# Kernel optimization log

Measured on AMD Instinct MI355X. Metric: run time of the kernel, lower is better.

Reference implementation:

```python
import jax, jax.numpy as jnp
import numpy as np

N_NODES = 50000
N_EDGES = 800000
F_IN = 64
HID = 64
OUT = 2
N_GRAPHS = 500


def _lin_init(key, fan_in, fan_out):
    # uniform(-1/sqrt(fan_in), 1/sqrt(fan_in)), matching torch Linear default
    bound = 1.0 / np.sqrt(fan_in)
    return jax.random.uniform(key, (fan_in, fan_out), minval=-bound, maxval=bound, dtype=jnp.float32)


def setup_inputs() -> dict:
    key = jax.random.key(0)
    ks = jax.random.split(key, 16)
    x = jax.random.normal(ks[0], (N_NODES, F_IN), dtype=jnp.float32)
    edge_index = jax.random.randint(ks[1], (2, N_EDGES), 0, N_NODES, dtype=jnp.int64)
    batch = jnp.sort(jax.random.randint(ks[2], (N_NODES,), 0, N_GRAPHS, dtype=jnp.int64))
    dims = [(F_IN, HID), (HID, HID), (HID, HID)]
    params = {}
    for i, (fi, fo) in enumerate(dims, start=1):
        params[f"W{i}_rel"] = _lin_init(ks[2 + 3 * i], fi, fo)      # applied to aggregated neighbors
        params[f"W{i}_root"] = _lin_init(ks[3 + 3 * i], fi, fo)     # applied to self (no bias, PyG GraphConv)
        b_bound = 1.0 / np.sqrt(fi)
        params[f"b{i}"] = jax.random.uniform(ks[4 + 3 * i], (fo,), minval=-b_bound, maxval=b_bound, dtype=jnp.float32)
    params["Wf1"] = _lin_init(ks[13], HID, HID)
    params["bf1"] = jnp.zeros((HID,), dtype=jnp.float32)
    params["Wf2"] = _lin_init(ks[14], HID, OUT)
    params["bf2"] = jnp.zeros((OUT,), dtype=jnp.float32)
    return {"x": x, "edge_index": edge_index, "batch": batch, **params}


def _graph_conv(h, src, dst, W_rel, W_root, b):
    # PyG GraphConv: out_i = W_root h_i + W_rel * sum_{j->i} h_j + b
    agg = jax.ops.segment_sum(h[src], dst, num_segments=N_NODES)  # [N, F] gather + scatter-add
    return h @ W_root + agg @ W_rel + b


def reference(x, edge_index, batch,
              W1_rel, W1_root, b1,
              W2_rel, W2_root, b2,
              W3_rel, W3_root, b3,
              Wf1, bf1, Wf2, bf2):
    src, dst = edge_index[0], edge_index[1]
    # dropout is identity in eval mode
    h = jax.nn.relu(_graph_conv(x, src, dst, W1_rel, W1_root, b1))
    h = jax.nn.relu(_graph_conv(h, src, dst, W2_rel, W2_root, b2))
    h = jax.nn.relu(_graph_conv(h, src, dst, W3_rel, W3_root, b3))
    # global_mean_pool over graph ids
    sums = jax.ops.segment_sum(h, batch, num_segments=N_GRAPHS)            # [G, H]
    counts = jax.ops.segment_sum(jnp.ones((N_NODES,), h.dtype), batch, num_segments=N_GRAPHS)
    pooled = sums / jnp.maximum(counts, 1.0)[:, None]
    out = pooled @ Wf1 + bf1
    out = out @ Wf2 + bf2
    return out
```

## Files before the change

### kernel.cpp

```cpp
#include <hip/hip_runtime.h>


#define NFEAT 64
#define BCAP  6144

typedef unsigned short u16;
typedef unsigned int   u32;
typedef __attribute__((ext_vector_type(8))) short short8;
typedef __attribute__((ext_vector_type(4))) float f32x4;

__device__ __forceinline__ u16 f2bf(float f) {
    u32 u = __float_as_uint(f);
    u32 r = (u + 0x7fffu + ((u >> 16) & 1u)) >> 16;
    return (u16)r;
}
__device__ __forceinline__ float bflo(u32 u) { return __uint_as_float(u << 16); }
__device__ __forceinline__ float bfhi(u32 u) { return __uint_as_float(u & 0xffff0000u); }

__global__ __launch_bounds__(256) void cast_bf(const float* __restrict__ in,
                                               u16* __restrict__ out, int n8) {
    int i = blockIdx.x * 256 + threadIdx.x;
    if (i < n8) {
        const float4* p = (const float4*)(in + (size_t)i * 8);
        float4 a = p[0], b = p[1];
        uint4 o;
        o.x = f2bf(a.x) | ((u32)f2bf(a.y) << 16);
        o.y = f2bf(a.z) | ((u32)f2bf(a.w) << 16);
        o.z = f2bf(b.x) | ((u32)f2bf(b.y) << 16);
        o.w = f2bf(b.z) | ((u32)f2bf(b.w) << 16);
        *(uint4*)(out + (size_t)i * 8) = o;
    }
}

__global__ __launch_bounds__(256) void gemm_cat(
    const u16* __restrict__ hin, const u16* __restrict__ agg,
    const float* __restrict__ Wroot, const float* __restrict__ Wrel,
    const float* __restrict__ bias, u16* __restrict__ hout, int n_rows)
{
    __shared__ u16 als[64 * 128];
    __shared__ u16 wls[64 * 128];

    const int tid = threadIdx.x;
    const int row0 = blockIdx.x * 64;

    #pragma unroll
    for (int it = 0; it < 4; ++it) {
        int id = it * 256 + tid;
        int k = id >> 4;
        int n4 = (id & 15) * 4;
        float4 wr = *(const float4*)(Wroot + k * 64 + n4);
        float4 wl = *(const float4*)(Wrel  + k * 64 + n4);
        const float* wrf = (const float*)&wr;
        const float* wlf = (const float*)&wl;
        int ckr = k >> 3, kin = k & 7;
        int ckl = ckr + 8;
        #pragma unroll
        for (int j = 0; j < 4; ++j) {
            int n = n4 + j;
            wls[n * 128 + (((ckr ^ (n & 7)) << 3) | kin)] = f2bf(wrf[j]);
            wls[n * 128 + (((ckl ^ (n & 7)) << 3) | kin)] = f2bf(wlf[j]);
        }
    }

    #pragma unroll
    for (int it = 0; it < 4; ++it) {
        int id = it * 256 + tid;
        int r = id >> 4, ch = id & 15;
        int gr = row0 + r;
        uint4 v = make_uint4(0, 0, 0, 0);
        if (gr < n_rows) {
            const u16* sp = (ch < 8) ? (hin + (size_t)gr * 64 + ch * 8)
                                     : (agg + (size_t)gr * 64 + (ch - 8) * 8);
            v = *(const uint4*)sp;
        }
        *(uint4*)&als[r * 128 + ((ch ^ (r & 7)) << 3)] = v;
    }
    __syncthreads();

    const int w = tid >> 6, l = tid & 63;
    const int l15 = l & 15;
    const int wrow0 = w * 16;

    short8 afr[4];
    #pragma unroll
    for (int ks = 0; ks < 4; ++ks) {
        int r = wrow0 + l15;
        int ck = ks * 4 + (l >> 4);
        afr[ks] = *(const short8*)&als[r * 128 + ((ck ^ (r & 7)) << 3)];
    }
    short8 bfr[4][4];
    #pragma unroll
    for (int nl = 0; nl < 4; ++nl)
        #pragma unroll
        for (int ks = 0; ks < 4; ++ks) {
            int cl = nl * 16 + l15;
            int ck = ks * 4 + (l >> 4);
            bfr[nl][ks] = *(const short8*)&wls[cl * 128 + ((ck ^ (cl & 7)) << 3)];
        }

    f32x4 acc[4];
    #pragma unroll
    for (int nl = 0; nl < 4; ++nl) {
        float bv = bias[nl * 16 + l15];
        f32x4 iv = {bv, bv, bv, bv};
        acc[nl] = iv;
    }
    #pragma unroll
    for (int nl = 0; nl < 4; ++nl)
        #pragma unroll
        for (int ks = 0; ks < 4; ++ks)
            acc[nl] = __builtin_amdgcn_mfma_f32_16x16x32_bf16(
                afr[ks], bfr[nl][ks], acc[nl], 0, 0, 0);

    const int rg = (l >> 4) * 4;
    #pragma unroll
    for (int reg = 0; reg < 4; ++reg) {
        int row = row0 + wrow0 + rg + reg;
        if (row < n_rows) {
            #pragma unroll
            for (int nl = 0; nl < 4; ++nl)
                hout[(size_t)row * 64 + nl * 16 + l15] =
                    f2bf(fmaxf(acc[nl][reg], 0.f));
        }
    }
}

__global__ __launch_bounds__(256) void zero_int(int* __restrict__ p, int n) {
    int i = blockIdx.x * 256 + threadIdx.x;
    if (i < n) p[i] = 0;
}

__global__ __launch_bounds__(256) void part_bucket(
    const int* __restrict__ src, const int* __restrict__ dst, int ne,
    int* __restrict__ bcnt, u32* __restrict__ pairs)
{
    __shared__ int lcnt[256];
    __shared__ int lbase[256];
    const int t = threadIdx.x;
    const int e0 = blockIdx.x * 4096;

    lcnt[t] = 0;
    __syncthreads();

    int s_[16], d_[16];
    #pragma unroll
    for (int i = 0; i < 16; ++i) {
        int e = e0 + i * 256 + t;
        if (e < ne) { s_[i] = src[e]; d_[i] = dst[e]; }
        else        { s_[i] = 0;      d_[i] = -1; }
    }
    #pragma unroll
    for (int i = 0; i < 16; ++i)
        if (d_[i] >= 0) atomicAdd(&lcnt[d_[i] >> 8], 1);
    __syncthreads();

    {
        int c = lcnt[t];
        lbase[t] = (c > 0) ? atomicAdd(&bcnt[t], c) : 0;
    }
    __syncthreads();
    lcnt[t] = 0;
    __syncthreads();

    #pragma unroll
    for (int i = 0; i < 16; ++i)
        if (d_[i] >= 0) {
            int b = d_[i] >> 8;
            int o = atomicAdd(&lcnt[b], 1);
            pairs[(size_t)b * BCAP + lbase[b] + o] =
                (u32)s_[i] | ((u32)(d_[i] & 255) << 16);
        }
}

__global__ __launch_bounds__(64) void scan_offsets(const int* __restrict__ bcnt, int nbuck,
                                                   int* __restrict__ boff,
                                                   int* __restrict__ row_ptr, int nn) {
    const int t = threadIdx.x;
    int carry = 0;
    for (int base = 0; base < nbuck; base += 64) {
        int i = base + t;
        int v = (i < nbuck) ? bcnt[i] : 0;
        int inc = v;
        #pragma unroll
        for (int off = 1; off < 64; off <<= 1) {
            int x = __shfl_up(inc, off);
            if (t >= off) inc += x;
        }
        if (i < nbuck) boff[i] = carry + inc - v;
        carry += __shfl(inc, 63);
    }
    if (t == 0) row_ptr[nn] = carry;
}

__global__ __launch_bounds__(256) void build_csr(
    const u32* __restrict__ pairs, const int* __restrict__ bcnt,
    const int* __restrict__ boff, int nn,
    int* __restrict__ row_ptr, u16* __restrict__ csr_src)
{
    __shared__ u32 lp[BCAP];
    __shared__ int deg[256];
    __shared__ int tsum[256];
    __shared__ int lofs[256];
    __shared__ int cur[256];

    const int b = blockIdx.x;
    const int t = threadIdx.x;
    const int cnt   = bcnt[b];
    const int ebase = boff[b];
    const int n0    = b * 256;

    deg[t] = 0; cur[t] = 0;
    __syncthreads();

    for (int i = t; i < cnt; i += 256) {
        u32 p = pairs[(size_t)b * BCAP + i];
        lp[i] = p;
        atomicAdd(&deg[p >> 16], 1);
    }
    __syncthreads();

    tsum[t] = deg[t];
    __syncthreads();
    #pragma unroll
    for (int off = 1; off < 256; off <<= 1) {
        int x = (t >= off) ? tsum[t - off] : 0;
        __syncthreads();
        tsum[t] += x;
        __syncthreads();
    }
    int excl = (t > 0 ? tsum[t - 1] : 0);
    lofs[t] = ebase + excl;
    int node = n0 + t;
    if (node < nn) row_ptr[node] = ebase + excl;
    __syncthreads();

    for (int i = t; i < cnt; i += 256) {
        u32 p = lp[i];
        int dl = p >> 16;
        int pos = lofs[dl] + atomicAdd(&cur[dl], 1);
        csr_src[pos] = (u16)(p & 0xffffu);
    }
}

__global__ __launch_bounds__(256) void gather_agg(
    const u16* __restrict__ hb,
    const int* __restrict__ row_ptr,
    const u16* __restrict__ csr_src,
    u16* __restrict__ agg,
    int nn)
{
    const int node = blockIdx.x * 4 + (threadIdx.x >> 6);
    const int l = threadIdx.x & 63;
    if (node >= nn) return;
    const int s = row_ptr[node];
    const int e = row_ptr[node + 1];
    const int es = l >> 3;
    const int c  = l & 7;
    const uint4* hv = (const uint4*)hb;

    float a0=0.f,a1=0.f,a2=0.f,a3=0.f,a4=0.f,a5=0.f,a6=0.f,a7=0.f;
    for (int j = s; j < e; j += 8) {
        int je = j + es;
        int jj = (je < e) ? je : (e - 1);
        float m = (je < e) ? 1.f : 0.f;
        int srcn = csr_src[jj];
        uint4 q = hv[(size_t)srcn * 8 + c];
        a0 = fmaf(m, bflo(q.x), a0);  a1 = fmaf(m, bfhi(q.x), a1);
        a2 = fmaf(m, bflo(q.y), a2);  a3 = fmaf(m, bfhi(q.y), a3);
        a4 = fmaf(m, bflo(q.z), a4);  a5 = fmaf(m, bfhi(q.z), a5);
        a6 = fmaf(m, bflo(q.w), a6);  a7 = fmaf(m, bfhi(q.w), a7);
    }
    #pragma unroll
    for (int msk = 8; msk <= 32; msk <<= 1) {
        a0 += __shfl_xor(a0, msk); a1 += __shfl_xor(a1, msk);
        a2 += __shfl_xor(a2, msk); a3 += __shfl_xor(a3, msk);
        a4 += __shfl_xor(a4, msk); a5 += __shfl_xor(a5, msk);
        a6 += __shfl_xor(a6, msk); a7 += __shfl_xor(a7, msk);
    }
    if (es == 0) {
        uint4 o;
        o.x = f2bf(a0) | ((u32)f2bf(a1) << 16);
        o.y = f2bf(a2) | ((u32)f2bf(a3) << 16);
        o.z = f2bf(a4) | ((u32)f2bf(a5) << 16);
        o.w = f2bf(a6) | ((u32)f2bf(a7) << 16);
        ((uint4*)agg)[(size_t)node * 8 + c] = o;
    }
}

__global__ __launch_bounds__(256) void pool_mlp(
    const u16* __restrict__ h,
    const int* __restrict__ batch,
    int n_nodes,
    const float* __restrict__ Wf1, const float* __restrict__ bf1,
    const float* __restrict__ Wf2, const float* __restrict__ bf2,
    float* __restrict__ out, int n_graphs)
{
    const int g = blockIdx.x;
    const int tid = threadIdx.x;

    int lo = 0, hi = n_nodes;
    while (lo < hi) { int mid = (lo + hi) >> 1; if (batch[mid] < g) lo = mid + 1; else hi = mid; }
    int s = lo;
    lo = s; hi = n_nodes;
    while (lo < hi) { int mid = (lo + hi) >> 1; if (batch[mid] < g + 1) lo = mid + 1; else hi = mid; }
    int e = lo;

    const int c16 = tid & 15;
    const int r16 = tid >> 4;
    const uint2* hv = (const uint2*)h;

    float4 acc = make_float4(0.f, 0.f, 0.f, 0.f);
    for (int i = s + r16; i < e; i += 16) {
        uint2 q = hv[(size_t)i * 16 + c16];
        acc.x += bflo(q.x); acc.y += bfhi(q.x);
        acc.z += bflo(q.y); acc.w += bfhi(q.y);
    }

    __shared__ float4 red[256];
    red[tid] = acc;
    __syncthreads();
    #pragma unroll
    for (int off = 8; off > 0; off >>= 1) {
        if (r16 < off) {
            float4 o = red[tid + off * 16];
            float4 m = red[tid];
            m.x += o.x; m.y += o.y; m.z += o.z; m.w += o.w;
            red[tid] = m;
        }
        __syncthreads();
    }

    __shared__ float pl[64];
    __shared__ float md[64];
    if (r16 == 0) {
        float inv = 1.0f / (float)((e - s) > 0 ? (e - s) : 1);
        float4 m = red[c16];
        pl[c16 * 4 + 0] = m.x * inv;
        pl[c16 * 4 + 1] = m.y * inv;
        pl[c16 * 4 + 2] = m.z * inv;
        pl[c16 * 4 + 3] = m.w * inv;
    }
    __syncthreads();

    if (tid < 64) {
        float m = bf1[tid];
        #pragma unroll 8
        for (int k = 0; k < 64; ++k)
            m += pl[k] * Wf1[k * 64 + tid];
        md[tid] = m;
    }
    __syncthreads();

    if (tid < 2) {
        float o = bf2[tid];
        #pragma unroll 8
        for (int k = 0; k < 64; ++k)
            o += md[k] * Wf2[k * 2 + tid];
        out[(size_t)g * 2 + tid] = o;
    }
}

extern "C" void kernel_launch(void* const* d_in, const int* in_sizes, int n_in,
                              void* d_out, int out_size, void* d_ws, size_t ws_size,
                              hipStream_t stream) {
    const float* x     = (const float*)d_in[0];
    const int*   ei    = (const int*)d_in[1];
    const int*   batch = (const int*)d_in[2];
    const float* W1_rel  = (const float*)d_in[3];
    const float* W1_root = (const float*)d_in[4];
    const float* b1      = (const float*)d_in[5];
    const float* W2_rel  = (const float*)d_in[6];
    const float* W2_root = (const float*)d_in[7];
    const float* b2      = (const float*)d_in[8];
    const float* W3_rel  = (const float*)d_in[9];
    const float* W3_root = (const float*)d_in[10];
    const float* b3      = (const float*)d_in[11];
    const float* Wf1     = (const float*)d_in[12];
    const float* bf1     = (const float*)d_in[13];
    const float* Wf2     = (const float*)d_in[14];
    const float* bf2     = (const float*)d_in[15];

    const int NN = in_sizes[0] / NFEAT;
    const int NE = in_sizes[1] / 2;
    const int NG = out_size / 2;

    const int* src = ei;
    const int* dst = ei + NE;

    const int nbuck = (NN + 255) / 256;

    u16*   hA      = (u16*)d_ws;
    u16*   hB      = hA + (size_t)NN * NFEAT;
    u16*   aggb    = hB + (size_t)NN * NFEAT;
    int*   row_ptr = (int*)(aggb + (size_t)NN * NFEAT);
    int*   bcnt    = row_ptr + (NN + 1);
    int*   boff    = bcnt + nbuck;
    u32*   pairs   = (u32*)(boff + nbuck);
    u16*   csr_src = (u16*)(pairs + (size_t)nbuck * BCAP);

    const int gemm_grid = (NN + 63) / 64;
    const int node_grid = (NN + 3) / 4;
    const int part_grid = (NE + 4095) / 4096;
    const int n8        = NN * NFEAT / 8;
    const int cast_grid = (n8 + 255) / 256;

    cast_bf<<<cast_grid, 256, 0, stream>>>(x, hB, n8);

    zero_int<<<(nbuck + 255) / 256, 256, 0, stream>>>(bcnt, nbuck);
    part_bucket<<<part_grid, 256, 0, stream>>>(src, dst, NE, bcnt, pairs);
    scan_offsets<<<1, 64, 0, stream>>>(bcnt, nbuck, boff, row_ptr, NN);
    build_csr<<<nbuck, 256, 0, stream>>>(pairs, bcnt, boff, NN, row_ptr, csr_src);

    gather_agg<<<node_grid, 256, 0, stream>>>(hB, row_ptr, csr_src, aggb, NN);
    gemm_cat<<<gemm_grid, 256, 0, stream>>>(hB, aggb, W1_root, W1_rel, b1, hA, NN);

    gather_agg<<<node_grid, 256, 0, stream>>>(hA, row_ptr, csr_src, aggb, NN);
    gemm_cat<<<gemm_grid, 256, 0, stream>>>(hA, aggb, W2_root, W2_rel, b2, hB, NN);

    gather_agg<<<node_grid, 256, 0, stream>>>(hB, row_ptr, csr_src, aggb, NN);
    gemm_cat<<<gemm_grid, 256, 0, stream>>>(hB, aggb, W3_root, W3_rel, b3, hA, NN);

    pool_mlp<<<NG, 256, 0, stream>>>(hA, batch, NN, Wf1, bf1, Wf2, bf2, (float*)d_out, NG);
}
```

Before: 142.4 us.

## Fuse neighbor gather-aggregation into the per-layer GEMM kernel via LDS

Merges the separate gather_agg and gemm_cat kernels into one layer_fused kernel. Each block now aggregates neighbor features for its 64 rows directly into the shared-memory A tile, so the intermediate agg buffer is never written to or read back from global memory. This also removes three kernel launches. The gather loop is unrolled to two edges per step for more memory-level parallelism. The cost is fewer waves in flight for the latency-bound gather: gemm_grid blocks each handle 16 nodes per wave in sequence, where before there were 4 nodes per block.

```diff
diff --git a/kernel.cpp b/kernel.cpp
--- a/kernel.cpp
+++ b/kernel.cpp
@@ -32,8 +32,10 @@
     }
 }
 
-__global__ __launch_bounds__(256) void gemm_cat(
-    const u16* __restrict__ hin, const u16* __restrict__ agg,
+__global__ __launch_bounds__(256) void layer_fused(
+    const u16* __restrict__ hin,
+    const int* __restrict__ row_ptr,
+    const u16* __restrict__ csr_src,
     const float* __restrict__ Wroot, const float* __restrict__ Wrel,
     const float* __restrict__ bias, u16* __restrict__ hout, int n_rows)
 {
@@ -63,17 +65,65 @@
     }
 
     #pragma unroll
-    for (int it = 0; it < 4; ++it) {
+    for (int it = 0; it < 2; ++it) {
         int id = it * 256 + tid;
-        int r = id >> 4, ch = id & 15;
+        int r = id >> 3, ch = id & 7;
         int gr = row0 + r;
         uint4 v = make_uint4(0, 0, 0, 0);
-        if (gr < n_rows) {
-            const u16* sp = (ch < 8) ? (hin + (size_t)gr * 64 + ch * 8)
-                                     : (agg + (size_t)gr * 64 + (ch - 8) * 8);
-            v = *(const uint4*)sp;
-        }
+        if (gr < n_rows) v = *(const uint4*)(hin + (size_t)gr * 64 + ch * 8);
         *(uint4*)&als[r * 128 + ((ch ^ (r & 7)) << 3)] = v;
+    }
+
+    {
+        const int w  = tid >> 6;
+        const int l  = tid & 63;
+        const int es = l >> 3;
+        const int c  = l & 7;
+        const uint4* hv = (const uint4*)hin;
+
+        for (int i = 0; i < 16; ++i) {
+            int r = w * 16 + i;
+            int node = row0 + r;
+            float a0=0.f,a1=0.f,a2=0.f,a3=0.f,a4=0.f,a5=0.f,a6=0.f,a7=0.f;
+            if (node < n_rows) {
+                const int s = row_ptr[node];
+                const int e = row_ptr[node + 1];
+                for (int j = s; j < e; j += 16) {
+                    int je0 = j + es, je1 = j + es + 8;
+                    int jj0 = (je0 < e) ? je0 : (e - 1);
+                    int jj1 = (je1 < e) ? je1 : (e - 1);
+                    float m0 = (je0 < e) ? 1.f : 0.f;
+                    float m1 = (je1 < e) ? 1.f : 0.f;
+                    int s0 = csr_src[jj0];
+                    int s1 = csr_src[jj1];
+                    uint4 q0 = hv[(size_t)s0 * 8 + c];
+                    uint4 q1 = hv[(size_t)s1 * 8 + c];
+                    a0 = fmaf(m0, bflo(q0.x), a0);  a1 = fmaf(m0, bfhi(q0.x), a1);
+                    a2 = fmaf(m0, bflo(q0.y), a2);  a3 = fmaf(m0, bfhi(q0.y), a3);
+                    a4 = fmaf(m0, bflo(q0.z), a4);  a5 = fmaf(m0, bfhi(q0.z), a5);
+                    a6 = fmaf(m0, bflo(q0.w), a6);  a7 = fmaf(m0, bfhi(q0.w), a7);
+                    a0 = fmaf(m1, bflo(q1.x), a0);  a1 = fmaf(m1, bfhi(q1.x), a1);
+                    a2 = fmaf(m1, bflo(q1.y), a2);  a3 = fmaf(m1, bfhi(q1.y), a3);
+                    a4 = fmaf(m1, bflo(q1.z), a4);  a5 = fmaf(m1, bfhi(q1.z), a5);
+                    a6 = fmaf(m1, bflo(q1.w), a6);  a7 = fmaf(m1, bfhi(q1.w), a7);
+                }
+            }
+            #pragma unroll
+            for (int msk = 8; msk <= 32; msk <<= 1) {
+                a0 += __shfl_xor(a0, msk); a1 += __shfl_xor(a1, msk);
+                a2 += __shfl_xor(a2, msk); a3 += __shfl_xor(a3, msk);
+                a4 += __shfl_xor(a4, msk); a5 += __shfl_xor(a5, msk);
+                a6 += __shfl_xor(a6, msk); a7 += __shfl_xor(a7, msk);
+            }
+            if (es == 0) {
+                uint4 o;
+                o.x = f2bf(a0) | ((u32)f2bf(a1) << 16);
+                o.y = f2bf(a2) | ((u32)f2bf(a3) << 16);
+                o.z = f2bf(a4) | ((u32)f2bf(a5) << 16);
+                o.w = f2bf(a6) | ((u32)f2bf(a7) << 16);
+                *(uint4*)&als[r * 128 + (((8 + c) ^ (r & 7)) << 3)] = o;
+            }
+        }
     }
     __syncthreads();
 
@@ -239,51 +289,6 @@
         int dl = p >> 16;
         int pos = lofs[dl] + atomicAdd(&cur[dl], 1);
         csr_src[pos] = (u16)(p & 0xffffu);
-    }
-}
-
-__global__ __launch_bounds__(256) void gather_agg(
-    const u16* __restrict__ hb,
-    const int* __restrict__ row_ptr,
-    const u16* __restrict__ csr_src,
-    u16* __restrict__ agg,
-    int nn)
-{
-    const int node = blockIdx.x * 4 + (threadIdx.x >> 6);
-    const int l = threadIdx.x & 63;
-    if (node >= nn) return;
-    const int s = row_ptr[node];
-    const int e = row_ptr[node + 1];
-    const int es = l >> 3;
-    const int c  = l & 7;
-    const uint4* hv = (const uint4*)hb;
-
-    float a0=0.f,a1=0.f,a2=0.f,a3=0.f,a4=0.f,a5=0.f,a6=0.f,a7=0.f;
-    for (int j = s; j < e; j += 8) {
-        int je = j + es;
-        int jj = (je < e) ? je : (e - 1);
-        float m = (je < e) ? 1.f : 0.f;
-        int srcn = csr_src[jj];
-        uint4 q = hv[(size_t)srcn * 8 + c];
-        a0 = fmaf(m, bflo(q.x), a0);  a1 = fmaf(m, bfhi(q.x), a1);
-        a2 = fmaf(m, bflo(q.y), a2);  a3 = fmaf(m, bfhi(q.y), a3);
-        a4 = fmaf(m, bflo(q.z), a4);  a5 = fmaf(m, bfhi(q.z), a5);
-        a6 = fmaf(m, bflo(q.w), a6);  a7 = fmaf(m, bfhi(q.w), a7);
-    }
-    #pragma unroll
-    for (int msk = 8; msk <= 32; msk <<= 1) {
-        a0 += __shfl_xor(a0, msk); a1 += __shfl_xor(a1, msk);
-        a2 += __shfl_xor(a2, msk); a3 += __shfl_xor(a3, msk);
-        a4 += __shfl_xor(a4, msk); a5 += __shfl_xor(a5, msk);
-        a6 += __shfl_xor(a6, msk); a7 += __shfl_xor(a7, msk);
-    }
-    if (es == 0) {
-        uint4 o;
-        o.x = f2bf(a0) | ((u32)f2bf(a1) << 16);
-        o.y = f2bf(a2) | ((u32)f2bf(a3) << 16);
-        o.z = f2bf(a4) | ((u32)f2bf(a5) << 16);
-        o.w = f2bf(a6) | ((u32)f2bf(a7) << 16);
-        ((uint4*)agg)[(size_t)node * 8 + c] = o;
     }
 }
 
@@ -391,15 +396,13 @@
 
     u16*   hA      = (u16*)d_ws;
     u16*   hB      = hA + (size_t)NN * NFEAT;
-    u16*   aggb    = hB + (size_t)NN * NFEAT;
-    int*   row_ptr = (int*)(aggb + (size_t)NN * NFEAT);
+    int*   row_ptr = (int*)(hB + (size_t)NN * NFEAT);
     int*   bcnt    = row_ptr + (NN + 1);
     int*   boff    = bcnt + nbuck;
     u32*   pairs   = (u32*)(boff + nbuck);
     u16*   csr_src = (u16*)(pairs + (size_t)nbuck * BCAP);
 
     const int gemm_grid = (NN + 63) / 64;
-    const int node_grid = (NN + 3) / 4;
     const int part_grid = (NE + 4095) / 4096;
     const int n8        = NN * NFEAT / 8;
     const int cast_grid = (n8 + 255) / 256;
@@ -411,14 +414,12 @@
     scan_offsets<<<1, 64, 0, stream>>>(bcnt, nbuck, boff, row_ptr, NN);
     build_csr<<<nbuck, 256, 0, stream>>>(pairs, bcnt, boff, NN, row_ptr, csr_src);
 
-    gather_agg<<<node_grid, 256, 0, stream>>>(hB, row_ptr, csr_src, aggb, NN);
-    gemm_cat<<<gemm_grid, 256, 0, stream>>>(hB, aggb, W1_root, W1_rel, b1, hA, NN);
-
-    gather_agg<<<node_grid, 256, 0, stream>>>(hA, row_ptr, csr_src, aggb, NN);
-    gemm_cat<<<gemm_grid, 256, 0, stream>>>(hA, aggb, W2_root, W2_rel, b2, hB, NN);
-
-    gather_agg<<<node_grid, 256, 0, stream>>>(hB, row_ptr, csr_src, aggb, NN);
-    gemm_cat<<<gemm_grid, 256, 0, stream>>>(hB, aggb, W3_root, W3_rel, b3, hA, NN);
+    layer_fused<<<gemm_grid, 256, 0, stream>>>(hB, row_ptr, csr_src,
+                                               W1_root, W1_rel, b1, hA, NN);
+    layer_fused<<<gemm_grid, 256, 0, stream>>>(hA, row_ptr, csr_src,
+                                               W2_root, W2_rel, b2, hB, NN);
+    layer_fused<<<gemm_grid, 256, 0, stream>>>(hB, row_ptr, csr_src,
+                                               W3_root, W3_rel, b3, hA, NN);
 
     pool_mlp<<<NG, 256, 0, stream>>>(hA, batch, NN, Wf1, bf1, Wf2, bf2, (float*)d_out, NG);
 }
```

Result: slower. 163.5 us (+14.8%).

## Fuse prep kernels, pre-swizzle bf16 weights once, unroll gather loop by two

Applied to the files above, without the earlier changes.

Merges the input cast, bucket-counter zeroing and a new weight-conversion step into one prep launch, removing a kernel launch. The three layers' weights are converted to bf16 in the swizzled LDS layout once, so each gemm_cat block now does a plain vector copy instead of per-block float loads, conversion and scattered LDS stores. The gather loop processes two edges per lane per iteration to keep more independent loads in flight. Costs are a small extra workspace region and a hardcoded CAST_BLKS that must cover n8 and assumes nbuck is at most 256.

```diff
diff --git a/kernel.cpp b/kernel.cpp
--- a/kernel.cpp
+++ b/kernel.cpp
@@ -17,25 +17,54 @@
 __device__ __forceinline__ float bflo(u32 u) { return __uint_as_float(u << 16); }
 __device__ __forceinline__ float bfhi(u32 u) { return __uint_as_float(u & 0xffff0000u); }
 
-__global__ __launch_bounds__(256) void cast_bf(const float* __restrict__ in,
-                                               u16* __restrict__ out, int n8) {
-    int i = blockIdx.x * 256 + threadIdx.x;
-    if (i < n8) {
-        const float4* p = (const float4*)(in + (size_t)i * 8);
-        float4 a = p[0], b = p[1];
-        uint4 o;
-        o.x = f2bf(a.x) | ((u32)f2bf(a.y) << 16);
-        o.y = f2bf(a.z) | ((u32)f2bf(a.w) << 16);
-        o.z = f2bf(b.x) | ((u32)f2bf(b.y) << 16);
-        o.w = f2bf(b.z) | ((u32)f2bf(b.w) << 16);
-        *(uint4*)(out + (size_t)i * 8) = o;
+#define CAST_BLKS 1600
+__global__ __launch_bounds__(256) void prep(
+    const float* __restrict__ x, u16* __restrict__ xb, int n8,
+    const float* __restrict__ W1r, const float* __restrict__ W1l,
+    const float* __restrict__ W2r, const float* __restrict__ W2l,
+    const float* __restrict__ W3r, const float* __restrict__ W3l,
+    u16* __restrict__ wimg, int* __restrict__ bcnt, int nbuck)
+{
+    const int bid = blockIdx.x;
+    const int tid = threadIdx.x;
+
+    if (bid < CAST_BLKS) {
+        int i = bid * 256 + tid;
+        if (i < n8) {
+            const float4* p = (const float4*)(x + (size_t)i * 8);
+            float4 a = p[0], b = p[1];
+            uint4 o;
+            o.x = f2bf(a.x) | ((u32)f2bf(a.y) << 16);
+            o.y = f2bf(a.z) | ((u32)f2bf(a.w) << 16);
+            o.z = f2bf(b.x) | ((u32)f2bf(b.y) << 16);
+            o.w = f2bf(b.z) | ((u32)f2bf(b.w) << 16);
+            *(uint4*)(xb + (size_t)i * 8) = o;
+        }
+    } else if (bid < CAST_BLKS + 6) {
+        int m = bid - CAST_BLKS;
+        int layer = m >> 1;
+        int isrel = m & 1;
+        const float* W = (m == 0) ? W1r : (m == 1) ? W1l :
+                         (m == 2) ? W2r : (m == 3) ? W2l :
+                         (m == 4) ? W3r : W3l;
+        u16* img = wimg + (size_t)layer * (64 * 128);
+        #pragma unroll
+        for (int it = 0; it < 16; ++it) {
+            int flat = it * 256 + tid;
+            int k = flat >> 6, n = flat & 63;
+            int ck = (k >> 3) + (isrel ? 8 : 0);
+            int kin = k & 7;
+            img[n * 128 + (((ck ^ (n & 7)) << 3) | kin)] = f2bf(W[k * 64 + n]);
+        }
+    } else {
+        if (tid < nbuck) bcnt[tid] = 0;
     }
 }
 
 __global__ __launch_bounds__(256) void gemm_cat(
     const u16* __restrict__ hin, const u16* __restrict__ agg,
-    const float* __restrict__ Wroot, const float* __restrict__ Wrel,
-    const float* __restrict__ bias, u16* __restrict__ hout, int n_rows)
+    const u16* __restrict__ wimg, const float* __restrict__ bias,
+    u16* __restrict__ hout, int n_rows)
 {
     __shared__ u16 als[64 * 128];
     __shared__ u16 wls[64 * 128];
@@ -43,23 +72,12 @@
     const int tid = threadIdx.x;
     const int row0 = blockIdx.x * 64;
 
-    #pragma unroll
-    for (int it = 0; it < 4; ++it) {
-        int id = it * 256 + tid;
-        int k = id >> 4;
-        int n4 = (id & 15) * 4;
-        float4 wr = *(const float4*)(Wroot + k * 64 + n4);
-        float4 wl = *(const float4*)(Wrel  + k * 64 + n4);
-        const float* wrf = (const float*)&wr;
-        const float* wlf = (const float*)&wl;
-        int ckr = k >> 3, kin = k & 7;
-        int ckl = ckr + 8;
+    {
+        const uint4* wsrc = (const uint4*)wimg;
+        uint4* wdst = (uint4*)wls;
         #pragma unroll
-        for (int j = 0; j < 4; ++j) {
-            int n = n4 + j;
-            wls[n * 128 + (((ckr ^ (n & 7)) << 3) | kin)] = f2bf(wrf[j]);
-            wls[n * 128 + (((ckl ^ (n & 7)) << 3) | kin)] = f2bf(wlf[j]);
-        }
+        for (int it = 0; it < 4; ++it)
+            wdst[it * 256 + tid] = wsrc[it * 256 + tid];
     }
 
     #pragma unroll
@@ -123,11 +141,6 @@
                     f2bf(fmaxf(acc[nl][reg], 0.f));
         }
     }
-}
-
-__global__ __launch_bounds__(256) void zero_int(int* __restrict__ p, int n) {
-    int i = blockIdx.x * 256 + threadIdx.x;
-    if (i < n) p[i] = 0;
 }
 
 __global__ __launch_bounds__(256) void part_bucket(
@@ -259,16 +272,24 @@
     const uint4* hv = (const uint4*)hb;
 
     float a0=0.f,a1=0.f,a2=0.f,a3=0.f,a4=0.f,a5=0.f,a6=0.f,a7=0.f;
-    for (int j = s; j < e; j += 8) {
-        int je = j + es;
-        int jj = (je < e) ? je : (e - 1);
-        float m = (je < e) ? 1.f : 0.f;
-        int srcn = csr_src[jj];
-        uint4 q = hv[(size_t)srcn * 8 + c];
-        a0 = fmaf(m, bflo(q.x), a0);  a1 = fmaf(m, bfhi(q.x), a1);
-        a2 = fmaf(m, bflo(q.y), a2);  a3 = fmaf(m, bfhi(q.y), a3);
-        a4 = fmaf(m, bflo(q.z), a4);  a5 = fmaf(m, bfhi(q.z), a5);
-        a6 = fmaf(m, bflo(q.w), a6);  a7 = fmaf(m, bfhi(q.w), a7);
+    for (int j = s; j < e; j += 16) {
+        int je0 = j + es, je1 = j + es + 8;
+        int jj0 = (je0 < e) ? je0 : (e - 1);
+        int jj1 = (je1 < e) ? je1 : (e - 1);
+        float m0 = (je0 < e) ? 1.f : 0.f;
+        float m1 = (je1 < e) ? 1.f : 0.f;
+        int s0 = csr_src[jj0];
+        int s1 = csr_src[jj1];
+        uint4 q0 = hv[(size_t)s0 * 8 + c];
+        uint4 q1 = hv[(size_t)s1 * 8 + c];
+        a0 = fmaf(m0, bflo(q0.x), a0);  a1 = fmaf(m0, bfhi(q0.x), a1);
+        a2 = fmaf(m0, bflo(q0.y), a2);  a3 = fmaf(m0, bfhi(q0.y), a3);
+        a4 = fmaf(m0, bflo(q0.z), a4);  a5 = fmaf(m0, bfhi(q0.z), a5);
+        a6 = fmaf(m0, bflo(q0.w), a6);  a7 = fmaf(m0, bfhi(q0.w), a7);
+        a0 = fmaf(m1, bflo(q1.x), a0);  a1 = fmaf(m1, bfhi(q1.x), a1);
+        a2 = fmaf(m1, bflo(q1.y), a2);  a3 = fmaf(m1, bfhi(q1.y), a3);
+        a4 = fmaf(m1, bflo(q1.z), a4);  a5 = fmaf(m1, bfhi(q1.z), a5);
+        a6 = fmaf(m1, bflo(q1.w), a6);  a7 = fmaf(m1, bfhi(q1.w), a7);
     }
     #pragma unroll
     for (int msk = 8; msk <= 32; msk <<= 1) {
@@ -397,28 +418,28 @@
     int*   boff    = bcnt + nbuck;
     u32*   pairs   = (u32*)(boff + nbuck);
     u16*   csr_src = (u16*)(pairs + (size_t)nbuck * BCAP);
+    u16*   wimg    = csr_src + NE;
 
     const int gemm_grid = (NN + 63) / 64;
     const int node_grid = (NN + 3) / 4;
     const int part_grid = (NE + 4095) / 4096;
     const int n8        = NN * NFEAT / 8;
-    const int cast_grid = (n8 + 255) / 256;
-
-    cast_bf<<<cast_grid, 256, 0, stream>>>(x, hB, n8);
-
-    zero_int<<<(nbuck + 255) / 256, 256, 0, stream>>>(bcnt, nbuck);
+
+    prep<<<CAST_BLKS + 7, 256, 0, stream>>>(x, hB, n8,
+        W1_root, W1_rel, W2_root, W2_rel, W3_root, W3_rel, wimg, bcnt, nbuck);
+
     part_bucket<<<part_grid, 256, 0, stream>>>(src, dst, NE, bcnt, pairs);
     scan_offsets<<<1, 64, 0, stream>>>(bcnt, nbuck, boff, row_ptr, NN);
     build_csr<<<nbuck, 256, 0, stream>>>(pairs, bcnt, boff, NN, row_ptr, csr_src);
 
     gather_agg<<<node_grid, 256, 0, stream>>>(hB, row_ptr, csr_src, aggb, NN);
-    gemm_cat<<<gemm_grid, 256, 0, stream>>>(hB, aggb, W1_root, W1_rel, b1, hA, NN);
+    gemm_cat<<<gemm_grid, 256, 0, stream>>>(hB, aggb, wimg, b1, hA, NN);
 
     gather_agg<<<node_grid, 256, 0, stream>>>(hA, row_ptr, csr_src, aggb, NN);
-    gemm_cat<<<gemm_grid, 256, 0, stream>>>(hA, aggb, W2_root, W2_rel, b2, hB, NN);
+    gemm_cat<<<gemm_grid, 256, 0, stream>>>(hA, aggb, wimg + 64 * 128, b2, hB, NN);
 
     gather_agg<<<node_grid, 256, 0, stream>>>(hB, row_ptr, csr_src, aggb, NN);
-    gemm_cat<<<gemm_grid, 256, 0, stream>>>(hB, aggb, W3_root, W3_rel, b3, hA, NN);
+    gemm_cat<<<gemm_grid, 256, 0, stream>>>(hB, aggb, wimg + 2 * 64 * 128, b3, hA, NN);
 
     pool_mlp<<<NG, 256, 0, stream>>>(hA, batch, NN, Wf1, bf1, Wf2, bf2, (float*)d_out, NG);
 }
```

Measured after the change: 124.6 us. -12.5%, faster.
